# Performance work log

Measured on AMD Instinct MI355X. Metric: run time of the kernel, lower is better.

The kernel has to match this reference:

```python
import jax, jax.numpy as jnp
import numpy as np

N_QUBITS = 6
N_LAYERS = 3
DIM = 2 ** N_QUBITS  # 64

# PauliZ sign table: signs[s, q] = +1 if bit q of basis state s is 0 else -1
# (wire 0 is the most-significant bit, matching pennylane default.qubit)
_IDX = np.arange(DIM)
SIGNS = np.stack([1.0 - 2.0 * ((_IDX >> (N_QUBITS - 1 - q)) & 1) for q in range(N_QUBITS)], axis=1).astype(np.float32)  # (64, 6)


def _rx_mat(theta):  # theta: (B,) -> (B,2,2) complex64
    c = jnp.cos(theta / 2).astype(jnp.complex64)
    s = (-1j * jnp.sin(theta / 2)).astype(jnp.complex64)
    return jnp.stack([jnp.stack([c, s], -1), jnp.stack([s, c], -1)], -2)


def _ry_mat(theta):  # theta: (B,) -> (B,2,2) complex64
    c = jnp.cos(theta / 2).astype(jnp.complex64)
    s = jnp.sin(theta / 2).astype(jnp.complex64)
    return jnp.stack([jnp.stack([c, -s], -1), jnp.stack([s, c], -1)], -2)


def _rz_mat(theta):  # theta: (B,) -> (B,2,2) complex64 (diagonal)
    z = jnp.zeros_like(theta).astype(jnp.complex64)
    e0 = jnp.exp(-1j * theta.astype(jnp.complex64) / 2)
    e1 = jnp.exp(1j * theta.astype(jnp.complex64) / 2)
    return jnp.stack([jnp.stack([e0, z], -1), jnp.stack([z, e1], -1)], -2)


def _apply_1q(state, U, w):
    # state: (B, 64); U: (B,2,2) batched or (2,2) shared; gate on wire w
    B = state.shape[0]
    st = state.reshape(B, 2 ** w, 2, 2 ** (N_QUBITS - 1 - w))
    if U.ndim == 3:
        st = jnp.einsum('bij,bajc->baic', U, st)
    else:
        st = jnp.einsum('ij,bajc->baic', U, st)
    return st.reshape(B, DIM)


def _cnot(state, c, t):
    # CNOT with control wire c, target wire t (fixed structure, batched over B)
    B = state.shape[0]
    s = state.reshape((B,) + (2,) * N_QUBITS)
    ac, at = c + 1, t + 1
    s0 = jnp.take(s, 0, axis=ac)
    s1 = jnp.take(s, 1, axis=ac)
    at2 = at - 1 if at > ac else at  # axis shift after removing control axis
    s1 = jnp.flip(s1, axis=at2)      # X on target when control == 1
    s = jnp.stack([s0, s1], axis=ac)
    return s.reshape(B, DIM)


def simulate(x6, q_weights):
    # x6: (B, 6) angles; q_weights: (3, 6). Returns PauliZ expvals (B, 6).
    B = x6.shape[0]
    state = jnp.zeros((B, DIM), dtype=jnp.complex64).at[:, 0].set(1.0)
    # input encoding: RX, RY, RZ on each wire with rolled input angles
    for i in range(N_QUBITS):
        state = _apply_1q(state, _rx_mat(x6[:, i % N_QUBITS]), i)
        state = _apply_1q(state, _ry_mat(x6[:, (i + 1) % N_QUBITS]), i)
        state = _apply_1q(state, _rz_mat(x6[:, (i + 2) % N_QUBITS]), i)
    # variational layers: RY(weights) then ring of CNOTs
    for l in range(N_LAYERS):
        for q in range(N_QUBITS):
            th = q_weights[l, q]
            c = jnp.cos(th / 2).astype(jnp.complex64)
            s = jnp.sin(th / 2).astype(jnp.complex64)
            U = jnp.stack([jnp.stack([c, -s]), jnp.stack([s, c])])  # (2,2)
            state = _apply_1q(state, U, q)
        for q in range(N_QUBITS):
            state = _cnot(state, q, (q + 1) % N_QUBITS)
    probs = (state.real ** 2 + state.imag ** 2)  # (B, 64) float32
    return probs @ jnp.asarray(SIGNS)            # (B, 6)


def setup_inputs() -> dict:
    key = jax.random.key(0)
    k1, k2, k3, k4 = jax.random.split(key, 4)
    B, H = 32768, 1024
    x = jax.random.normal(k1, (B, N_QUBITS), dtype=jnp.float32)
    hx = jax.random.normal(k2, (B, H), dtype=jnp.float32)
    q_weights = jax.random.uniform(k3, (N_LAYERS, N_QUBITS), dtype=jnp.float32, minval=0.0, maxval=2.0 * np.pi)
    bound = 1.0 / np.sqrt(N_QUBITS)
    fc_w = jax.random.uniform(k4, (H, N_QUBITS), dtype=jnp.float32, minval=-bound, maxval=bound)
    fc_b = jax.random.uniform(jax.random.fold_in(k4, 1), (H,), dtype=jnp.float32, minval=-bound, maxval=bound)
    return {"x": x, "hx": hx, "q_weights": q_weights, "fc_w": fc_w, "fc_b": fc_b}


def reference(x, hx, q_weights, fc_w, fc_b):
    q = simulate(x[:, :N_QUBITS], q_weights)      # (B, 6) PauliZ expvals
    return hx + q @ fc_w.T + fc_b                 # residual + linear
```

## Files before the change

### kernel.cpp

```cpp
#include <hip/hip_runtime.h>


#define NQ 6
#define DIM 64

struct Perm { int v[DIM]; };
constexpr Perm make_perm() {
    Perm p{};
    for (int s = 0; s < DIM; ++s) {
        int src = s;
        for (int q = 5; q >= 0; --q) {
            int cb = 5 - q;
            int tb = 5 - ((q + 1) % 6);
            src ^= ((src >> cb) & 1) << tb;
        }
        p.v[s] = src;
    }
    return p;
}
constexpr Perm PS = make_perm();

template<int BB>
__device__ __forceinline__ void rx_gate(float* sr, float* si, float c, float sn) {
    constexpr int m = 1 << BB;
    #pragma unroll
    for (int p = 0; p < 32; ++p) {
        const int s0 = ((p & ~(m - 1)) << 1) | (p & (m - 1));
        const int s1 = s0 | m;
        float a0r = sr[s0], a0i = si[s0], a1r = sr[s1], a1i = si[s1];
        sr[s0] = c * a0r + sn * a1i;
        si[s0] = c * a0i - sn * a1r;
        sr[s1] = c * a1r + sn * a0i;
        si[s1] = c * a1i - sn * a0r;
    }
}

template<int BB>
__device__ __forceinline__ void ry_gate(float* sr, float* si, float c, float sn) {
    constexpr int m = 1 << BB;
    #pragma unroll
    for (int p = 0; p < 32; ++p) {
        const int s0 = ((p & ~(m - 1)) << 1) | (p & (m - 1));
        const int s1 = s0 | m;
        float a0r = sr[s0], a0i = si[s0], a1r = sr[s1], a1i = si[s1];
        sr[s0] = c * a0r - sn * a1r;
        si[s0] = c * a0i - sn * a1i;
        sr[s1] = sn * a0r + c * a1r;
        si[s1] = sn * a0i + c * a1i;
    }
}

template<int BB>
__device__ __forceinline__ void rz_gate(float* sr, float* si, float c, float sn) {
    constexpr int m = 1 << BB;
    #pragma unroll
    for (int s = 0; s < DIM; ++s) {
        float r = sr[s], i2 = si[s];
        if (s & m) { sr[s] = c * r - sn * i2;  si[s] = c * i2 + sn * r; }
        else       { sr[s] = c * r + sn * i2;  si[s] = c * i2 - sn * r; }
    }
}

__device__ __forceinline__ void cnot_ring(float* sr, float* si) {
    float tr[DIM], ti[DIM];
    #pragma unroll
    for (int s = 0; s < DIM; ++s) { tr[s] = sr[PS.v[s]]; ti[s] = si[PS.v[s]]; }
    #pragma unroll
    for (int s = 0; s < DIM; ++s) { sr[s] = tr[s]; si[s] = ti[s]; }
}

__global__ __launch_bounds__(64, 1) void qrnn_sim_kernel(
    const float* __restrict__ x,
    const float* __restrict__ qw,
    float* __restrict__ q6,
    int B)
{
    const int b = blockIdx.x * 64 + threadIdx.x;
    if (b >= B) return;

    float cx[6], sx[6];
    #pragma unroll
    for (int i = 0; i < 6; ++i)
        __sincosf(x[(size_t)b * 6 + i] * 0.5f, &sx[i], &cx[i]);

    float sr[DIM], si[DIM];
    #pragma unroll
    for (int s = 0; s < DIM; ++s) { sr[s] = (s == 0) ? 1.0f : 0.0f; si[s] = 0.0f; }

    #define ENC_WIRE(i) \
        rx_gate<5-(i)>(sr, si, cx[(i)],       sx[(i)]); \
        ry_gate<5-(i)>(sr, si, cx[((i)+1)%6], sx[((i)+1)%6]); \
        rz_gate<5-(i)>(sr, si, cx[((i)+2)%6], sx[((i)+2)%6]);
    ENC_WIRE(0) ENC_WIRE(1) ENC_WIRE(2) ENC_WIRE(3) ENC_WIRE(4) ENC_WIRE(5)
    #undef ENC_WIRE

    #define VAR_GATE(l, q) { \
        float c, s2; __sincosf(qw[(l)*6+(q)] * 0.5f, &s2, &c); \
        ry_gate<5-(q)>(sr, si, c, s2); }
    #define VAR_LAYER(l) \
        VAR_GATE(l,0) VAR_GATE(l,1) VAR_GATE(l,2) \
        VAR_GATE(l,3) VAR_GATE(l,4) VAR_GATE(l,5) \
        cnot_ring(sr, si);
    VAR_LAYER(0) VAR_LAYER(1) VAR_LAYER(2)
    #undef VAR_LAYER
    #undef VAR_GATE

    float q[6] = {0.f, 0.f, 0.f, 0.f, 0.f, 0.f};
    #pragma unroll
    for (int s = 0; s < DIM; ++s) {
        float p = sr[s] * sr[s] + si[s] * si[s];
        #pragma unroll
        for (int j = 0; j < 6; ++j)
            q[j] += (s & (1 << (5 - j))) ? -p : p;
    }
    #pragma unroll
    for (int j = 0; j < 6; ++j) q6[(size_t)b * 6 + j] = q[j];
}

#define NB 16
#define BATCH 8

__global__ __launch_bounds__(256) void qrnn_epi_kernel(
    const float* __restrict__ hx,
    const float* __restrict__ q6,
    const float* __restrict__ fc_w,
    const float* __restrict__ fc_b,
    float* __restrict__ out,
    int H)
{
    const int h4 = threadIdx.x;
    const int b0 = blockIdx.x * NB;

    __shared__ float q6s[NB][6];
    if (threadIdx.x < NB * 6)
        q6s[threadIdx.x / 6][threadIdx.x % 6] = q6[(size_t)b0 * 6 + threadIdx.x];

    const float4* w4 = (const float4*)fc_w;
    const int wb = h4 * 6;
    float4 a0 = w4[wb + 0], a1 = w4[wb + 1], a2 = w4[wb + 2];
    float4 a3 = w4[wb + 3], a4 = w4[wb + 4], a5 = w4[wb + 5];
    float4 bv = ((const float4*)fc_b)[h4];
    __syncthreads();

    #pragma unroll
    for (int t = 0; t < NB / BATCH; ++t) {
        float4 hv[BATCH];
        #pragma unroll
        for (int r = 0; r < BATCH; ++r)
            hv[r] = ((const float4*)(hx + (size_t)(b0 + t * BATCH + r) * H))[h4];
        #pragma unroll
        for (int r = 0; r < BATCH; ++r) {
            const float* qb = q6s[t * BATCH + r];
            float q0 = qb[0], q1 = qb[1], q2 = qb[2];
            float q3 = qb[3], q4 = qb[4], q5 = qb[5];
            float4 res;
            res.x = hv[r].x + bv.x + q0*a0.x + q1*a0.y + q2*a0.z + q3*a0.w + q4*a1.x + q5*a1.y;
            res.y = hv[r].y + bv.y + q0*a1.z + q1*a1.w + q2*a2.x + q3*a2.y + q4*a2.z + q5*a2.w;
            res.z = hv[r].z + bv.z + q0*a3.x + q1*a3.y + q2*a3.z + q3*a3.w + q4*a4.x + q5*a4.y;
            res.w = hv[r].w + bv.w + q0*a4.z + q1*a4.w + q2*a5.x + q3*a5.y + q4*a5.z + q5*a5.w;
            ((float4*)(out + (size_t)(b0 + t * BATCH + r) * H))[h4] = res;
        }
    }
}

extern "C" void kernel_launch(void* const* d_in, const int* in_sizes, int n_in,
                              void* d_out, int out_size, void* d_ws, size_t ws_size,
                              hipStream_t stream) {
    const float* x    = (const float*)d_in[0];
    const float* hx   = (const float*)d_in[1];
    const float* qw   = (const float*)d_in[2];
    const float* fc_w = (const float*)d_in[3];
    const float* fc_b = (const float*)d_in[4];
    float* out = (float*)d_out;

    const int B = in_sizes[0] / NQ;
    const int H = in_sizes[4];

    float* q6 = (float*)d_ws;

    qrnn_sim_kernel<<<(B + 63) / 64, 64, 0, stream>>>(x, qw, q6, B);
    qrnn_epi_kernel<<<B / NB, H / 4, 0, stream>>>(hx, q6, fc_w, fc_b, out, H);
}
```

Baseline: 262.0 us.

## Fuse simulation and epilogue into one kernel with wave-distributed statevector

Replaces the per-thread 64-amplitude statevector simulation with a wave-level layout in which each lane holds one amplitude and gates are applied through cross-lane shuffles. The quantum simulation and the residual-plus-linear epilogue are merged into a single kernel, so the q6 workspace round trip and the second launch go away. The hx loads are issued before the simulation so their latency can overlap it, and outputs use nontemporal stores. In exchange, H=1024 and the batch size are hardcoded into the indexing, and each sample now costs many shuffles.

Result: faster. 244.8 us (-6.6%).

```diff
diff --git a/kernel.cpp b/kernel.cpp
--- a/kernel.cpp
+++ b/kernel.cpp
@@ -2,164 +2,121 @@
 
 
 #define NQ 6
-#define DIM 64
 
-struct Perm { int v[DIM]; };
-constexpr Perm make_perm() {
-    Perm p{};
-    for (int s = 0; s < DIM; ++s) {
-        int src = s;
-        for (int q = 5; q >= 0; --q) {
-            int cb = 5 - q;
-            int tb = 5 - ((q + 1) % 6);
-            src ^= ((src >> cb) & 1) << tb;
-        }
-        p.v[s] = src;
-    }
-    return p;
-}
-constexpr Perm PS = make_perm();
+typedef float floatx4 __attribute__((ext_vector_type(4)));
 
-template<int BB>
-__device__ __forceinline__ void rx_gate(float* sr, float* si, float c, float sn) {
-    constexpr int m = 1 << BB;
-    #pragma unroll
-    for (int p = 0; p < 32; ++p) {
-        const int s0 = ((p & ~(m - 1)) << 1) | (p & (m - 1));
-        const int s1 = s0 | m;
-        float a0r = sr[s0], a0i = si[s0], a1r = sr[s1], a1i = si[s1];
-        sr[s0] = c * a0r + sn * a1i;
-        si[s0] = c * a0i - sn * a1r;
-        sr[s1] = c * a1r + sn * a0i;
-        si[s1] = c * a1i - sn * a0r;
-    }
-}
+__global__ __launch_bounds__(256, 4) void qrnn_fused_kernel(
+    const float* __restrict__ x,
+    const float* __restrict__ hx,
+    const float* __restrict__ qw,
+    const float* __restrict__ fc_w,
+    const float* __restrict__ fc_b,
+    float* __restrict__ out)
+{
+    const int tid = threadIdx.x;
+    const int l   = tid & 63;
+    const int wv  = tid >> 6;
+    const int bid = blockIdx.x;
+    const int G   = gridDim.x;
 
-template<int BB>
-__device__ __forceinline__ void ry_gate(float* sr, float* si, float c, float sn) {
-    constexpr int m = 1 << BB;
-    #pragma unroll
-    for (int p = 0; p < 32; ++p) {
-        const int s0 = ((p & ~(m - 1)) << 1) | (p & (m - 1));
-        const int s1 = s0 | m;
-        float a0r = sr[s0], a0i = si[s0], a1r = sr[s1], a1i = si[s1];
-        sr[s0] = c * a0r - sn * a1r;
-        si[s0] = c * a0i - sn * a1i;
-        sr[s1] = sn * a0r + c * a1r;
-        si[s1] = sn * a0i + c * a1i;
-    }
-}
+    __shared__ float q6s[4][6];
 
-template<int BB>
-__device__ __forceinline__ void rz_gate(float* sr, float* si, float c, float sn) {
-    constexpr int m = 1 << BB;
-    #pragma unroll
-    for (int s = 0; s < DIM; ++s) {
-        float r = sr[s], i2 = si[s];
-        if (s & m) { sr[s] = c * r - sn * i2;  si[s] = c * i2 + sn * r; }
-        else       { sr[s] = c * r + sn * i2;  si[s] = c * i2 - sn * r; }
-    }
-}
+    const float4* hx4 = (const float4*)hx;
+    float4 hv0 = hx4[(size_t)(bid + 0 * G) * 256 + tid];
+    float4 hv1 = hx4[(size_t)(bid + 1 * G) * 256 + tid];
+    float4 hv2 = hx4[(size_t)(bid + 2 * G) * 256 + tid];
+    float4 hv3 = hx4[(size_t)(bid + 3 * G) * 256 + tid];
+    const float4* w4 = (const float4*)fc_w;
+    const int wb = tid * 6;
+    float4 a0 = w4[wb + 0], a1 = w4[wb + 1], a2 = w4[wb + 2];
+    float4 a3 = w4[wb + 3], a4 = w4[wb + 4], a5 = w4[wb + 5];
+    float4 bv = ((const float4*)fc_b)[tid];
 
-__device__ __forceinline__ void cnot_ring(float* sr, float* si) {
-    float tr[DIM], ti[DIM];
-    #pragma unroll
-    for (int s = 0; s < DIM; ++s) { tr[s] = sr[PS.v[s]]; ti[s] = si[PS.v[s]]; }
-    #pragma unroll
-    for (int s = 0; s < DIM; ++s) { sr[s] = tr[s]; si[s] = ti[s]; }
-}
+    const int b = bid + wv * G;
 
-__global__ __launch_bounds__(64, 1) void qrnn_sim_kernel(
-    const float* __restrict__ x,
-    const float* __restrict__ qw,
-    float* __restrict__ q6,
-    int B)
-{
-    const int b = blockIdx.x * 64 + threadIdx.x;
-    if (b >= B) return;
+    float ang = 0.f;
+    if (l < 6)        ang = x[(size_t)b * NQ + l];
+    else if (l < 24)  ang = qw[l - 6];
+    float sa, ca;
+    __sincosf(ang * 0.5f, &sa, &ca);
 
     float cx[6], sx[6];
     #pragma unroll
-    for (int i = 0; i < 6; ++i)
-        __sincosf(x[(size_t)b * 6 + i] * 0.5f, &sx[i], &cx[i]);
+    for (int i = 0; i < 6; ++i) { cx[i] = __shfl(ca, i); sx[i] = __shfl(sa, i); }
 
-    float sr[DIM], si[DIM];
+    float re = (l == 0) ? 1.f : 0.f;
+    float im = 0.f;
+
     #pragma unroll
-    for (int s = 0; s < DIM; ++s) { sr[s] = (s == 0) ? 1.0f : 0.0f; si[s] = 0.0f; }
+    for (int w = 0; w < 6; ++w) {
+        const int m = 1 << (5 - w);
+        const float sgn = (l & m) ? 1.f : -1.f;
+        float pr = __shfl_xor(re, m), pi = __shfl_xor(im, m);
+        float c = cx[w], s = sx[w];
+        float nr = c * re + s * pi;
+        float ni = c * im - s * pr;
+        re = nr; im = ni;
+        pr = __shfl_xor(re, m); pi = __shfl_xor(im, m);
+        c = cx[(w + 1) % 6]; s = sx[(w + 1) % 6] * sgn;
+        nr = c * re + s * pr;
+        ni = c * im + s * pi;
+        re = nr; im = ni;
+        c = cx[(w + 2) % 6];
+        const float sg = (l & m) ? -sx[(w + 2) % 6] : sx[(w + 2) % 6];
+        nr = c * re + sg * im;
+        ni = c * im - sg * re;
+        re = nr; im = ni;
+    }
 
-    #define ENC_WIRE(i) \
-        rx_gate<5-(i)>(sr, si, cx[(i)],       sx[(i)]); \
-        ry_gate<5-(i)>(sr, si, cx[((i)+1)%6], sx[((i)+1)%6]); \
-        rz_gate<5-(i)>(sr, si, cx[((i)+2)%6], sx[((i)+2)%6]);
-    ENC_WIRE(0) ENC_WIRE(1) ENC_WIRE(2) ENC_WIRE(3) ENC_WIRE(4) ENC_WIRE(5)
-    #undef ENC_WIRE
+    int src = l;
+    #pragma unroll
+    for (int q = 5; q >= 0; --q) {
+        const int cb = 5 - q, tb = 5 - ((q + 1) % 6);
+        src ^= ((src >> cb) & 1) << tb;
+    }
 
-    #define VAR_GATE(l, q) { \
-        float c, s2; __sincosf(qw[(l)*6+(q)] * 0.5f, &s2, &c); \
-        ry_gate<5-(q)>(sr, si, c, s2); }
-    #define VAR_LAYER(l) \
-        VAR_GATE(l,0) VAR_GATE(l,1) VAR_GATE(l,2) \
-        VAR_GATE(l,3) VAR_GATE(l,4) VAR_GATE(l,5) \
-        cnot_ring(sr, si);
-    VAR_LAYER(0) VAR_LAYER(1) VAR_LAYER(2)
-    #undef VAR_LAYER
-    #undef VAR_GATE
+    #pragma unroll
+    for (int lay = 0; lay < 3; ++lay) {
+        #pragma unroll
+        for (int q = 0; q < 6; ++q) {
+            const int m = 1 << (5 - q);
+            const float c = __shfl(ca, 6 + lay * 6 + q);
+            const float s = __shfl(sa, 6 + lay * 6 + q);
+            const float sg = (l & m) ? s : -s;
+            const float pr = __shfl_xor(re, m), pi = __shfl_xor(im, m);
+            const float nr = c * re + sg * pr;
+            const float ni = c * im + sg * pi;
+            re = nr; im = ni;
+        }
+        re = __shfl(re, src);
+        im = __shfl(im, src);
+    }
 
-    float q[6] = {0.f, 0.f, 0.f, 0.f, 0.f, 0.f};
+    float p = re * re + im * im;
     #pragma unroll
-    for (int s = 0; s < DIM; ++s) {
-        float p = sr[s] * sr[s] + si[s] * si[s];
-        #pragma unroll
-        for (int j = 0; j < 6; ++j)
-            q[j] += (s & (1 << (5 - j))) ? -p : p;
+    for (int k = 0; k < 6; ++k) {
+        const int m = 1 << k;
+        const float t = __shfl_xor(p, m);
+        p = (l & m) ? (t - p) : (t + p);
     }
-    #pragma unroll
-    for (int j = 0; j < 6; ++j) q6[(size_t)b * 6 + j] = q[j];
-}
-
-#define NB 16
-#define BATCH 8
-
-__global__ __launch_bounds__(256) void qrnn_epi_kernel(
-    const float* __restrict__ hx,
-    const float* __restrict__ q6,
-    const float* __restrict__ fc_w,
-    const float* __restrict__ fc_b,
-    float* __restrict__ out,
-    int H)
-{
-    const int h4 = threadIdx.x;
-    const int b0 = blockIdx.x * NB;
-
-    __shared__ float q6s[NB][6];
-    if (threadIdx.x < NB * 6)
-        q6s[threadIdx.x / 6][threadIdx.x % 6] = q6[(size_t)b0 * 6 + threadIdx.x];
-
-    const float4* w4 = (const float4*)fc_w;
-    const int wb = h4 * 6;
-    float4 a0 = w4[wb + 0], a1 = w4[wb + 1], a2 = w4[wb + 2];
-    float4 a3 = w4[wb + 3], a4 = w4[wb + 4], a5 = w4[wb + 5];
-    float4 bv = ((const float4*)fc_b)[h4];
+    const int srcl = (l < 6) ? (32 >> l) : 0;
+    const float v = __shfl(p, srcl);
+    if (l < 6) q6s[wv][l] = v;
     __syncthreads();
 
+    floatx4* out4 = (floatx4*)out;
     #pragma unroll
-    for (int t = 0; t < NB / BATCH; ++t) {
-        float4 hv[BATCH];
-        #pragma unroll
-        for (int r = 0; r < BATCH; ++r)
-            hv[r] = ((const float4*)(hx + (size_t)(b0 + t * BATCH + r) * H))[h4];
-        #pragma unroll
-        for (int r = 0; r < BATCH; ++r) {
-            const float* qb = q6s[t * BATCH + r];
-            float q0 = qb[0], q1 = qb[1], q2 = qb[2];
-            float q3 = qb[3], q4 = qb[4], q5 = qb[5];
-            float4 res;
-            res.x = hv[r].x + bv.x + q0*a0.x + q1*a0.y + q2*a0.z + q3*a0.w + q4*a1.x + q5*a1.y;
-            res.y = hv[r].y + bv.y + q0*a1.z + q1*a1.w + q2*a2.x + q3*a2.y + q4*a2.z + q5*a2.w;
-            res.z = hv[r].z + bv.z + q0*a3.x + q1*a3.y + q2*a3.z + q3*a3.w + q4*a4.x + q5*a4.y;
-            res.w = hv[r].w + bv.w + q0*a4.z + q1*a4.w + q2*a5.x + q3*a5.y + q4*a5.z + q5*a5.w;
-            ((float4*)(out + (size_t)(b0 + t * BATCH + r) * H))[h4] = res;
-        }
+    for (int k = 0; k < 4; ++k) {
+        const float* qb = q6s[k];
+        const float q0 = qb[0], q1 = qb[1], q2 = qb[2];
+        const float q3 = qb[3], q4 = qb[4], q5 = qb[5];
+        const float4 hvk = (k == 0) ? hv0 : (k == 1) ? hv1 : (k == 2) ? hv2 : hv3;
+        floatx4 res;
+        res.x = hvk.x + bv.x + q0*a0.x + q1*a0.y + q2*a0.z + q3*a0.w + q4*a1.x + q5*a1.y;
+        res.y = hvk.y + bv.y + q0*a1.z + q1*a1.w + q2*a2.x + q3*a2.y + q4*a2.z + q5*a2.w;
+        res.z = hvk.z + bv.z + q0*a3.x + q1*a3.y + q2*a3.z + q3*a3.w + q4*a4.x + q5*a4.y;
+        res.w = hvk.w + bv.w + q0*a4.z + q1*a4.w + q2*a5.x + q3*a5.y + q4*a5.z + q5*a5.w;
+        __builtin_nontemporal_store(res, &out4[(size_t)(bid + k * G) * 256 + tid]);
     }
 }
 
@@ -174,10 +131,6 @@
     float* out = (float*)d_out;
 
     const int B = in_sizes[0] / NQ;
-    const int H = in_sizes[4];
 
-    float* q6 = (float*)d_ws;
-
-    qrnn_sim_kernel<<<(B + 63) / 64, 64, 0, stream>>>(x, qw, q6, B);
-    qrnn_epi_kernel<<<B / NB, H / 4, 0, stream>>>(hx, q6, fc_w, fc_b, out, H);
+    qrnn_fused_kernel<<<B / 4, 256, 0, stream>>>(x, hx, qw, fc_w, fc_b, out);
 }
```
